# Kernel tuning notes

Hardware: AMD Instinct MI355X
Metric: run time of the kernel (lower is better)

Reference implementation:

```python
import jax, jax.numpy as jnp
import numpy as np

B, N, H = 512, 128, 256      # graphs, nodes per graph, hidden
NH, HD = 8, 32               # heads, head dim
DEG = 8
E = B * N * DEG              # 524288 edges
BN_EPS = 1e-5


def setup_inputs() -> dict:
    key = jax.random.key(0)
    ks = jax.random.split(key, 16)

    def w(k, shape):
        return jax.random.normal(k, shape, dtype=jnp.float32) * 0.02

    # intra-graph random edges: base offset per graph, local src/dst in [0, N)
    base = jnp.repeat(jnp.arange(B, dtype=jnp.int32) * N, N * DEG)
    edge_src = base + jax.random.randint(ks[1], (E,), 0, N, dtype=jnp.int32)
    edge_dst = base + jax.random.randint(ks[2], (E,), 0, N, dtype=jnp.int32)

    return {
        "h": jax.random.normal(ks[0], (B * N, H), dtype=jnp.float32),
        "edge_src": edge_src,
        "edge_dst": edge_dst,
        "gin_w1": w(ks[3], (H, H)), "gin_b1": jnp.zeros((H,), jnp.float32),
        "gin_w2": w(ks[4], (H, H)), "gin_b2": jnp.zeros((H,), jnp.float32),
        "attn_in_w": w(ks[5], (3 * H, H)), "attn_in_b": jnp.zeros((3 * H,), jnp.float32),
        "attn_out_w": w(ks[6], (H, H)), "attn_out_b": jnp.zeros((H,), jnp.float32),
        "bn_local_g": jnp.ones((H,), jnp.float32), "bn_local_b": jnp.zeros((H,), jnp.float32),
        "bn_attn_g": jnp.ones((H,), jnp.float32), "bn_attn_b": jnp.zeros((H,), jnp.float32),
        "bn_out_g": jnp.ones((H,), jnp.float32), "bn_out_b": jnp.zeros((H,), jnp.float32),
        "ffn1_w": w(ks[7], (2 * H, H)), "ffn1_b": jnp.zeros((2 * H,), jnp.float32),
        "ffn2_w": w(ks[8], (H, 2 * H)), "ffn2_b": jnp.zeros((H,), jnp.float32),
    }


def _bn(x, g, b):
    # nn.BatchNorm1d training-mode forward: batch stats over node dim, biased var
    mean = jnp.mean(x, axis=0)
    var = jnp.mean(jnp.square(x - mean), axis=0)
    return g * (x - mean) * jax.lax.rsqrt(var + BN_EPS) + b


def _mha(x, in_w, in_b, out_w, out_b):
    # x: [B, N, H]; uniform graphs -> key_padding_mask is all-valid
    qkv = x @ in_w.T + in_b                           # [B, N, 3H]
    q, k, v = jnp.split(qkv, 3, axis=-1)
    def heads(t):
        return t.reshape(B, N, NH, HD).transpose(0, 2, 1, 3)  # [B, NH, N, HD]
    q, k, v = heads(q), heads(k), heads(v)
    scores = jnp.einsum('bhqd,bhkd->bhqk', q, k) / jnp.sqrt(jnp.float32(HD))
    att = jax.nn.softmax(scores, axis=-1)
    o = jnp.einsum('bhqk,bhkd->bhqd', att, v).transpose(0, 2, 1, 3).reshape(B, N, H)
    return o @ out_w.T + out_b


def reference(h, edge_src, edge_dst,
              gin_w1, gin_b1, gin_w2, gin_b2,
              attn_in_w, attn_in_b, attn_out_w, attn_out_b,
              bn_local_g, bn_local_b, bn_attn_g, bn_attn_b, bn_out_g, bn_out_b,
              ffn1_w, ffn1_b, ffn2_w, ffn2_b):
    # --- local GIN branch: (1+eps)*h + sum_{j in N(i)} h_j, eps=0, then 2-layer MLP
    agg = jax.ops.segment_sum(h[edge_src], edge_dst, num_segments=B * N)
    z = h + agg
    h_local = jax.nn.relu(z @ gin_w1.T + gin_b1) @ gin_w2.T + gin_b2
    h_local = _bn(h + h_local, bn_local_g, bn_local_b)

    # --- global attention branch (to_dense_batch is an exact reshape here)
    h_dense = h.reshape(B, N, H)
    h_attn = _mha(h_dense, attn_in_w, attn_in_b, attn_out_w, attn_out_b).reshape(B * N, H)
    h_attn = _bn(h + h_attn, bn_attn_g, bn_attn_b)

    # --- combine + FFN + out norm
    x = h_local + h_attn
    x = x + jax.nn.relu(x @ ffn1_w.T + ffn1_b) @ ffn2_w.T + ffn2_b
    return _bn(x, bn_out_g, bn_out_b)
```

## Files before the change

### kernel.cpp

```cpp
#include <hip/hip_runtime.h>
#include <hip/hip_bf16.h>

#define B_   512
#define N_   128
#define H_   256
#define NH_  8
#define HD_  32
#define DEG_ 8
#define R_   (B_ * N_)
#define E_   (B_ * N_ * DEG_)
#define EPG_ (N_ * DEG_)

typedef unsigned short u16;
typedef unsigned int u32;

typedef __attribute__((ext_vector_type(8))) short s16x8;
typedef __attribute__((ext_vector_type(4))) float f32x4;

__device__ __forceinline__ float b2f(u16 u) {
  union { u32 i; float f; } v;
  v.i = ((u32)u) << 16;
  return v.f;
}
__device__ __forceinline__ u16 f2b(float f) {
// ... 33 lines not shown
#define OFF_F2B 657408
#define W_TOTAL 657664

__global__ __launch_bounds__(256) void prep_kernel(
    const float* __restrict__ hsrc, u16* __restrict__ hdst,
    const float* s0, const float* s1, const float* s2, const float* s3,
    const float* s4, const float* s5, const float* s6, const float* s7,
    const float* s8, const float* s9, const float* s10, const float* s11,
    u16* __restrict__ wdst, float* __restrict__ stats) {
  const int b = blockIdx.x, t = threadIdx.x;
  if (b < 16384) {
    const int e = (b * 256 + t) * 4;
    const float4 v = *(const float4*)(hsrc + e);
    ushort4 o;
    o.x = f2b(v.x); o.y = f2b(v.y); o.z = f2b(v.z); o.w = f2b(v.w);
    *(ushort4*)(hdst + tix(e >> 8, e & 255)) = o;
  } else if (b < 16384 + 643) {
    const int sizes[12] = {65536, 256, 65536, 256, 196608, 768,
                           65536, 256, 131072, 512, 131072, 256};
    const float* srcs[12] = {s0, s1, s2, s3, s4, s5, s6, s7, s8, s9, s10, s11};
    int gid = ((b - 16384) * 256 + t) * 4;
    if (gid >= W_TOTAL) return;
    int seg = 0, off = gid;
    while (off >= sizes[seg]) { off -= sizes[seg]; seg++; }
    const float4 v = *(const float4*)(srcs[seg] + off);
    ushort4 o;
    o.x = f2b(v.x); o.y = f2b(v.y); o.z = f2b(v.z); o.w = f2b(v.w);
    *(ushort4*)(wdst + gid) = o;
  } else {
    stats[(b - (16384 + 643)) * 256 + t] = 0.f;
  }
}

#define SROWS_ 32

__global__ __launch_bounds__(256) void agg_kernel(
    const u16* __restrict__ h, const int* __restrict__ esrc,
    const int* __restrict__ edst, u16* __restrict__ z) {
  __shared__ int s_src[EPG_];
  __shared__ int s_cnt[SROWS_];
  __shared__ int s_off[SROWS_ + 1];
  __shared__ int s_pos[SROWS_];
  const int g = blockIdx.x;
  const int r0 = blockIdx.y * SROWS_;
  const int t = threadIdx.x;

  if (t < SROWS_) s_cnt[t] = 0;
  __syncthreads();

  const int ebase = g * EPG_;
  int dl[4], sg[4];
#pragma unroll
  for (int i = 0; i < 4; i++) {
    const int e = ebase + t + i * 256;
    sg[i] = esrc[e];
    dl[i] = edst[e] - g * N_ - r0;
    if ((unsigned)dl[i] < SROWS_) atomicAdd(&s_cnt[dl[i]], 1);
  }
  __syncthreads();
  if (t == 0) {
    int acc = 0;
#pragma unroll
    for (int i = 0; i < SROWS_; i++) { s_off[i] = acc; acc += s_cnt[i]; }
    s_off[SROWS_] = acc;
  }
  __syncthreads();
  if (t < SROWS_) s_pos[t] = s_off[t];
  __syncthreads();
#pragma unroll
  for (int i = 0; i < 4; i++) {
    if ((unsigned)dl[i] < SROWS_) {
      const int slot = atomicAdd(&s_pos[dl[i]], 1);
      s_src[slot] = sg[i];
    }
  }
  __syncthreads();

  const int rg = t >> 5;
  const int c0 = (t & 31) * 8;
  for (int ib = 0; ib < SROWS_; ib += 8) {
    const int i = ib + rg;
    const int row = g * N_ + r0 + i;
    float acc[8];
    {
      const s16x8 v = *(const s16x8*)(h + tix(row, c0));
#pragma unroll
      for (int j = 0; j < 8; j++) acc[j] = b2f((u16)v[j]);
    }
    const int e0 = s_off[i], e1 = s_off[i + 1];
    for (int e = e0; e < e1; e++) {
      const int src = s_src[e];
      const s16x8 v = *(const s16x8*)(h + tix(src, c0));
#pragma unroll
      for (int j = 0; j < 8; j++) acc[j] += b2f((u16)v[j]);
    }
    s16x8 o;
#pragma unroll
    for (int j = 0; j < 8; j++) o[j] = (short)f2b(acc[j]);
    *(s16x8*)(z + tix(row, c0)) = o;
  }
}

template <int NC, int K, int RELU, int RES, int STATS, int ASPLIT, int CMODE>
__global__ __launch_bounds__(256) void gemm_mfma(
    const u16* A, const u16* A2,
    const u16* __restrict__ W, const u16* __restrict__ bias,
    const u16* res, u16* C0, u16* C1, u16* C2,
    float* __restrict__ gsum, float* __restrict__ gsq) {
  __shared__ u16 As[2][64 * 64] __attribute__((aligned(16)));
  __shared__ u16 Bs[2][64 * 64] __attribute__((aligned(16)));

  const int t = threadIdx.x;
  const int wave = t >> 6, lane = t & 63;
  const int wr = wave >> 1, wc = wave & 1;
  const int quad = lane >> 4, ln15 = lane & 15;
  const int row0 = blockIdx.y * 64, col0 = blockIdx.x * 64;

  f32x4 acc[2][2];
#pragma unroll
  for (int i = 0; i < 2; i++)
#pragma unroll
    for (int j = 0; j < 2; j++) acc[i][j] = (f32x4){0.f, 0.f, 0.f, 0.f};

  auto stage = [&](int b, int kt) {
    const u16* Ab;
    int ksl;
    if (ASPLIT) {
      if (kt < 256) { Ab = A; ksl = kt >> 6; } else { Ab = A2; ksl = (kt - 256) >> 6; }
    } else {
      Ab = A; ksl = kt >> 6;
    }
    const u16* abase = Ab + ((size_t)(row0 >> 7) << 15) + (ksl << 13) +
                       ((row0 & 64) << 6);
#pragma unroll
    for (int i = 0; i < 2; i++) {
      const int fid = t + i * 256;
      glds16(abase + fid * 8, &As[b][fid * 8]);
      const int row = fid >> 3;
      const int segp = (fid & 7) ^ (row & 7);
      glds16(W + (size_t)(col0 + row) * K + kt + segp * 8, &Bs[b][fid * 8]);
    }
  };

  stage(0, 0);
  for (int kt = 0; kt < K; kt += 64) {
    const int cur = (kt >> 6) & 1;
    if (kt + 64 < K) {
      stage(cur ^ 1, kt + 64);
      asm volatile("s_waitcnt vmcnt(4)" ::: "memory");
    } else {
      asm volatile("s_waitcnt vmcnt(0)" ::: "memory");
    }
    __builtin_amdgcn_s_barrier();
#pragma unroll
    for (int ks = 0; ks < 64; ks += 32) {
      s16x8 af[2], bf[2];
#pragma unroll
      for (int i = 0; i < 2; i++) {
        const int ra = wr * 32 + i * 16 + ln15;
        af[i] = *(const s16x8*)(
            &As[cur][ra * 64 + ((((ks >> 3) + quad) ^ (ra & 7)) * 8)]);
      }
#pragma unroll
      for (int j = 0; j < 2; j++) {
        const int rb = wc * 32 + j * 16 + ln15;
        bf[j] = *(const s16x8*)(
            &Bs[cur][rb * 64 + ((((ks >> 3) + quad) ^ (rb & 7)) * 8)]);
      }
#pragma unroll
      for (int i = 0; i < 2; i++)
#pragma unroll
        for (int j = 0; j < 2; j++)
          acc[i][j] = __builtin_amdgcn_mfma_f32_16x16x32_bf16(af[i], bf[j], acc[i][j], 0, 0, 0);
    }
    __builtin_amdgcn_s_barrier();
  }

  const int cbase = col0 + wc * 32;
  u16* Cb;
  int coff;
  if (CMODE) {
    const int chunk = col0 >> 8;
    Cb = (chunk == 0) ? C0 : ((chunk == 1) ? C1 : C2);
    coff = (col0 & 255) + wc * 32;
  } else {
    Cb = C0; coff = cbase;
  }

  float bs[2];
#pragma unroll
  for (int j = 0; j < 2; j++) bs[j] = b2f(bias[cbase + j * 16 + ln15]);

  float ssum[2] = {}, ssq[2] = {};
#pragma unroll
  for (int i = 0; i < 2; i++) {
    const int rbase = row0 + wr * 32 + i * 16 + quad * 4;
#pragma unroll
    for (int reg = 0; reg < 4; reg++) {
      const int row = rbase + reg;
#pragma unroll
      for (int j = 0; j < 2; j++) {
        float val = acc[i][j][reg] + bs[j];
        if (RELU) val = fmaxf(val, 0.f);
        if (RES) val += b2f(res[tix(row, cbase + j * 16 + ln15)]);
        Cb[tix(row, coff + j * 16 + ln15)] = f2b(val);
        if (STATS) { ssum[j] += val; ssq[j] += val * val; }
      }
    }
  }

  if (STATS) {
#pragma unroll
    for (int j = 0; j < 2; j++) {
      float s = ssum[j];
      s += __shfl_xor(s, 16);
      s += __shfl_xor(s, 32);
      float q = ssq[j];
      q += __shfl_xor(q, 16);
      q += __shfl_xor(q, 32);
      if (lane < 16) {
        atomicAdd(&gsum[cbase + j * 16 + lane], s);
        atomicAdd(&gsq[cbase + j * 16 + lane], q);
      }
    }
  }
}

__global__ __launch_bounds__(256) void qkv_mfma(
    const u16* A, const u16* __restrict__ W, const u16* __restrict__ bias,
    u16* Cq, u16* Ck, u16* Cv) {
  __shared__ u16 As[2][64 * 64] __attribute__((aligned(16)));
  __shared__ u16 Bs[2][3 * 64 * 64] __attribute__((aligned(16)));

  const int t = threadIdx.x;
  const int wave = t >> 6, lane = t & 63;
  const int wr = wave >> 1, wc = wave & 1;
  const int quad = lane >> 4, ln15 = lane & 15;
  const int row0 = blockIdx.y * 64, col0 = blockIdx.x * 64;

  f32x4 acc[3][2][2];
#pragma unroll
  for (int o = 0; o < 3; o++)
#pragma unroll
    for (int i = 0; i < 2; i++)
#pragma unroll
      for (int j = 0; j < 2; j++) acc[o][i][j] = (f32x4){0.f, 0.f, 0.f, 0.f};

  auto stage = [&](int b, int kt) {
    const u16* abase = A + ((size_t)(row0 >> 7) << 15) + ((kt >> 6) << 13) +
                       ((row0 & 64) << 6);
#pragma unroll
    for (int i = 0; i < 2; i++) {
      const int fid = t + i * 256;
      glds16(abase + fid * 8, &As[b][fid * 8]);
    }
#pragma unroll
    for (int o = 0; o < 3; o++)
#pragma unroll
      for (int i = 0; i < 2; i++) {
        const int fid = t + i * 256;
        const int row = fid >> 3;
        const int segp = (fid & 7) ^ (row & 7);
        glds16(W + (size_t)(o * 256 + col0 + row) * 256 + kt + segp * 8,
               &Bs[b][o * 4096 + fid * 8]);
      }
  };

  stage(0, 0);
  for (int kt = 0; kt < 256; kt += 64) {
    const int cur = (kt >> 6) & 1;
    if (kt + 64 < 256) {
      stage(cur ^ 1, kt + 64);
      asm volatile("s_waitcnt vmcnt(8)" ::: "memory");
    } else {
      asm volatile("s_waitcnt vmcnt(0)" ::: "memory");
    }
    __builtin_amdgcn_s_barrier();
#pragma unroll
    for (int ks = 0; ks < 64; ks += 32) {
      s16x8 af[2];
#pragma unroll
      for (int i = 0; i < 2; i++) {
        const int ra = wr * 32 + i * 16 + ln15;
        af[i] = *(const s16x8*)(
            &As[cur][ra * 64 + ((((ks >> 3) + quad) ^ (ra & 7)) * 8)]);
      }
#pragma unroll
      for (int o = 0; o < 3; o++) {
        s16x8 bf[2];
#pragma unroll
        for (int j = 0; j < 2; j++) {
          const int rb = wc * 32 + j * 16 + ln15;
          bf[j] = *(const s16x8*)(
              &Bs[cur][o * 4096 + rb * 64 + ((((ks >> 3) + quad) ^ (rb & 7)) * 8)]);
        }
#pragma unroll
        for (int i = 0; i < 2; i++)
#pragma unroll
          for (int j = 0; j < 2; j++)
            acc[o][i][j] = __builtin_amdgcn_mfma_f32_16x16x32_bf16(af[i], bf[j], acc[o][i][j], 0, 0, 0);
      }
    }
    __builtin_amdgcn_s_barrier();
  }

  const int cbase = col0 + wc * 32;
#pragma unroll
  for (int o = 0; o < 3; o++) {
    u16* Co = (o == 0) ? Cq : ((o == 1) ? Ck : Cv);
    float bs[2];
#pragma unroll
    for (int j = 0; j < 2; j++) bs[j] = b2f(bias[o * 256 + cbase + j * 16 + ln15]);
#pragma unroll
    for (int i = 0; i < 2; i++) {
      const int rbase = row0 + wr * 32 + i * 16 + quad * 4;
#pragma unroll
      for (int reg = 0; reg < 4; reg++) {
        const int row = rbase + reg;
#pragma unroll
        for (int j = 0; j < 2; j++)
          Co[tix(row, cbase + j * 16 + ln15)] = f2b(acc[o][i][j][reg] + bs[j]);
      }
    }
  }
}

template <int CHUNKS, int RES_LDS, int COMBINE>
__global__ __launch_bounds__(256, 2) void fused_mlp(
    const u16* A, const u16* Ara,
    const u16* __restrict__ W1, const u16* __restrict__ b1,
    const u16* __restrict__ W2, const u16* __restrict__ b2,
    const u16* resg, u16* C, const float* __restrict__ st,
    const float* __restrict__ bn0g, const float* __restrict__ bn0b,
    const float* __restrict__ bn1g, const float* __restrict__ bn1b,
    float* __restrict__ gsum, float* __restrict__ gsq) {
  __shared__ u16 xs[4 * 64 * 64] __attribute__((aligned(16)));
  __shared__ u16 tc[64 * 128] __attribute__((aligned(16)));
  __shared__ u16 Wst[2][128 * 64] __attribute__((aligned(16)));

  const int t = threadIdx.x;
  const int wave = t >> 6, lane = t & 63;
  const int wr = wave >> 1, wc = wave & 1;
  const int quad = lane >> 4, ln15 = lane & 15;
  const int row0 = blockIdx.x * 64;
  const int K2 = CHUNKS * 128;

  if (COMBINE) {
    float* cf = (float*)tc;
    {
      const float ml = st[t] * (1.f / R_);
      const float vl = fmaxf(st[256 + t] * (1.f / R_) - ml * ml, 0.f);
      const float al = bn0g[t] * rsqrtf(vl + 1e-5f);
      cf[t] = al;
      cf[256 + t] = bn0b[t] - ml * al;
// ... 177 lines not shown
      const int rowl = wr * 32 + i * 16 + quad * 4 + reg;
      const int row = row0 + rowl;
#pragma unroll
      for (int j = 0; j < 8; j++) {
        const int col = wc * 128 + j * 16 + ln15;
        float val = acc2[i][j][reg] + bs2[j];
        if (RES_LDS) {
          val += b2f(xs[(col >> 6) * 4096 + rowl * 64 +
                        ((((col >> 3) & 7) ^ (rowl & 7)) << 3) + (col & 7)]);
        } else {
          val += b2f(resg[tix(row, col)]);
        }
        C[tix(row, col)] = f2b(val);
        ssum[j] += val; ssq[j] += val * val;
      }
    }
  }

#pragma unroll
  for (int j = 0; j < 8; j++) {
    float s = ssum[j];
    s += __shfl_xor(s, 16);
    s += __shfl_xor(s, 32);
    float q = ssq[j];
    q += __shfl_xor(q, 16);
    q += __shfl_xor(q, 32);
    if (lane < 16) {
      atomicAdd(&gsum[wc * 128 + j * 16 + lane], s);
      atomicAdd(&gsq[wc * 128 + j * 16 + lane], q);
    }
  }
}

__global__ __launch_bounds__(256) void attn_mfma(
    const u16* q, const u16* __restrict__ k,
    const u16* __restrict__ v, u16* o) {
  __shared__ u16 lds[21760] __attribute__((aligned(16)));
  u16* Vt = lds;
  u16* Qs = lds + 4352;
  u16* Ks = lds + 4352 + 5120;
  u16* P  = lds + 4352;

  const int g = blockIdx.x >> 3;
  const int hd = blockIdx.x & 7;
  const int t = threadIdx.x;
  const int wave = t >> 6, lane = t & 63;
  const int quad = lane >> 4, ln15 = lane & 15;
  const int strip = wave * 32;
  const float scale = 0.1767766952966369f;

#pragma unroll
  for (int i = 0; i < 4; i++) {
    const int fid = t + i * 256;
    const int row = fid >> 3;
    const int seg = fid & 7;
    const int gidx = tix(g * N_ + row, hd * HD_ + seg * 4);
    const ushort4 qv = *(const ushort4*)(q + gidx);
    const ushort4 kv = *(const ushort4*)(k + gidx);
    const ushort4 vv = *(const ushort4*)(v + gidx);
    ushort4 qs;
    qs.x = f2b(b2f(qv.x) * scale); qs.y = f2b(b2f(qv.y) * scale);
    qs.z = f2b(b2f(qv.z) * scale); qs.w = f2b(b2f(qv.w) * scale);
    *(ushort4*)(Qs + row * 40 + seg * 4) = qs;
    *(ushort4*)(Ks + row * 40 + seg * 4) = kv;
    Vt[(seg * 4 + 0) * 136 + row] = vv.x;
    Vt[(seg * 4 + 1) * 136 + row] = vv.y;
    Vt[(seg * 4 + 2) * 136 + row] = vv.z;
    Vt[(seg * 4 + 3) * 136 + row] = vv.w;
  }
  __syncthreads();

  s16x8 af[2], bf[8];
#pragma unroll
  for (int mi = 0; mi < 2; mi++)
    af[mi] = *(const s16x8*)(Qs + (strip + mi * 16 + ln15) * 40 + quad * 8);
#pragma unroll
  for (int nj = 0; nj < 8; nj++)
    bf[nj] = *(const s16x8*)(Ks + (nj * 16 + ln15) * 40 + quad * 8);

  f32x4 acc[2][8];
#pragma unroll
  for (int mi = 0; mi < 2; mi++)
#pragma unroll
    for (int nj = 0; nj < 8; nj++)
      acc[mi][nj] = __builtin_amdgcn_mfma_f32_16x16x32_bf16(
          af[mi], bf[nj], (f32x4){0.f, 0.f, 0.f, 0.f}, 0, 0, 0);

  __syncthreads();

#pragma unroll
  for (int mi = 0; mi < 2; mi++) {
#pragma unroll
    for (int reg = 0; reg < 4; reg++) {
      float mx = acc[mi][0][reg];
#pragma unroll
      for (int j = 1; j < 8; j++) mx = fmaxf(mx, acc[mi][j][reg]);
      mx = fmaxf(mx, __shfl_xor(mx, 1));
      mx = fmaxf(mx, __shfl_xor(mx, 2));
      mx = fmaxf(mx, __shfl_xor(mx, 4));
      mx = fmaxf(mx, __shfl_xor(mx, 8));
      float e[8], s = 0.f;
#pragma unroll
      for (int j = 0; j < 8; j++) { e[j] = __expf(acc[mi][j][reg] - mx); s += e[j]; }
      s += __shfl_xor(s, 1);
      s += __shfl_xor(s, 2);
      s += __shfl_xor(s, 4);
      s += __shfl_xor(s, 8);
      const float inv = 1.f / s;
      const int prow = strip + mi * 16 + quad * 4 + reg;
#pragma unroll
      for (int j = 0; j < 8; j++)
        P[prow * 136 + j * 16 + ln15] = f2b(e[j] * inv);
    }
  }
  __syncthreads();

  f32x4 acc2[2][2];
#pragma unroll
  for (int mi = 0; mi < 2; mi++)
#pragma unroll
    for (int nj = 0; nj < 2; nj++) acc2[mi][nj] = (f32x4){0.f, 0.f, 0.f, 0.f};
#pragma unroll
  for (int kt = 0; kt < 4; kt++) {
    s16x8 paf[2], vbf[2];
#pragma unroll
    for (int mi = 0; mi < 2; mi++)
      paf[mi] = *(const s16x8*)(P + (strip + mi * 16 + ln15) * 136 + kt * 32 + quad * 8);
#pragma unroll
    for (int nj = 0; nj < 2; nj++)
      vbf[nj] = *(const s16x8*)(Vt + (nj * 16 + ln15) * 136 + kt * 32 + quad * 8);
#pragma unroll
    for (int mi = 0; mi < 2; mi++)
#pragma unroll
      for (int nj = 0; nj < 2; nj++)
        acc2[mi][nj] = __builtin_amdgcn_mfma_f32_16x16x32_bf16(
            paf[mi], vbf[nj], acc2[mi][nj], 0, 0, 0);
  }

#pragma unroll
  for (int mi = 0; mi < 2; mi++)
#pragma unroll
    for (int nj = 0; nj < 2; nj++)
#pragma unroll
      for (int reg = 0; reg < 4; reg++) {
        const int row = strip + mi * 16 + quad * 4 + reg;
        o[tix(g * N_ + row, hd * HD_ + nj * 16 + ln15)] =
            f2b(acc2[mi][nj][reg]);
      }
}

__global__ __launch_bounds__(256) void final_kernel(
    const u16* __restrict__ y, const float* __restrict__ st,
    const float* __restrict__ bg, const float* __restrict__ bb,
    float* __restrict__ out) {
  const int e = (blockIdx.x * 256 + threadIdx.x) * 4;
  const int col = e & 255;
  float y4[4];
  ld4b(y + tix(e >> 8, col), y4);
  const float4 s4 = *(const float4*)(st + 1024 + col);
  const float4 q4 = *(const float4*)(st + 1280 + col);
  const float4 g4 = *(const float4*)(bg + col);
  const float4 b4 = *(const float4*)(bb + col);
  const float ss[4] = {s4.x, s4.y, s4.z, s4.w};
  const float qq[4] = {q4.x, q4.y, q4.z, q4.w};
  const float gg[4] = {g4.x, g4.y, g4.z, g4.w};
  const float bv[4] = {b4.x, b4.y, b4.z, b4.w};
  float4 o;
  float* ov = (float*)&o;
#pragma unroll
  for (int j = 0; j < 4; j++) {
    const float mean = ss[j] * (1.f / R_);
    const float var = fmaxf(qq[j] * (1.f / R_) - mean * mean, 0.f);
    const float a = gg[j] * rsqrtf(var + 1e-5f);
    ov[j] = a * y4[j] + (bv[j] - mean * a);
  }
  *(float4*)(out + e) = o;
}

extern "C" void kernel_launch(void* const* d_in, const int* in_sizes, int n_in,
                              void* d_out, int out_size, void* d_ws, size_t ws_size,
                              hipStream_t stream) {
  const float* h = (const float*)d_in[0];
  const int* esrc = (const int*)d_in[1];
  const int* edst = (const int*)d_in[2];
  const float* bn_local_g = (const float*)d_in[11];
  const float* bn_local_b = (const float*)d_in[12];
  const float* bn_attn_g = (const float*)d_in[13];
  const float* bn_attn_b = (const float*)d_in[14];
  const float* bn_out_g = (const float*)d_in[15];
  const float* bn_out_b = (const float*)d_in[16];

  const size_t RH = (size_t)R_ * H_;
  float* stats = (float*)d_ws;
  u16* WB = (u16*)((char*)d_ws + 65536);
  u16* Hb = (u16*)((char*)d_ws + 65536 + 2097152);
  u16* S1 = Hb + RH;
  u16* S2 = S1 + RH;
  u16* OD = (u16*)d_out;
  float* outf = (float*)d_out;

  prep_kernel<<<16384 + 643 + 12, 256, 0, stream>>>(
      h, Hb,
      (const float*)d_in[3], (const float*)d_in[4], (const float*)d_in[5],
      (const float*)d_in[6], (const float*)d_in[7], (const float*)d_in[8],
      (const float*)d_in[9], (const float*)d_in[10], (const float*)d_in[17],
      (const float*)d_in[18], (const float*)d_in[19], (const float*)d_in[20],
      WB, stats);

  qkv_mfma<<<dim3(4, 1024), 256, 0, stream>>>(
      Hb, WB + OFF_AIW, WB + OFF_AIB, S1, S2, OD);
  attn_mfma<<<B_ * NH_, 256, 0, stream>>>(S1, S2, OD, S1);
  gemm_mfma<256, 256, 0, 1, 1, 0, 0><<<dim3(4, 1024), 256, 0, stream>>>(
      S1, nullptr, WB + OFF_AOW, WB + OFF_AOB, Hb, S2, nullptr, nullptr,
      stats + 512, stats + 768);
  agg_kernel<<<dim3(B_, 4), 256, 0, stream>>>(Hb, esrc, edst, OD);
  fused_mlp<2, 0, 0><<<1024, 256, 0, stream>>>(
      OD, nullptr,
      WB + OFF_GW1, WB + OFF_GB1, WB + OFF_GW2, WB + OFF_GB2,
      Hb, OD, nullptr, nullptr, nullptr, nullptr, nullptr,
      stats + 0, stats + 256);
  fused_mlp<4, 1, 1><<<1024, 256, 0, stream>>>(
      OD, S2,
      WB + OFF_F1W, WB + OFF_F1B, WB + OFF_F2W, WB + OFF_F2B,
      nullptr, S1, stats, bn_local_g, bn_local_b, bn_attn_g, bn_attn_b,
      stats + 1024, stats + 1280);
  final_kernel<<<(int)(RH / 4 / 256), 256, 0, stream>>>(
      S1, stats, bn_out_g, bn_out_b, outf);
}
```

Measured before the change: 532.5 us.

## Merge independent branch kernels into horizontally fused launches

Attention and GIN neighbor aggregation now share one launch that dispatches on block index, and the GIN MLP and attention output projection share a second launch. Aggregation output goes to a separate buffer (OD2) so the two branches no longer conflict over OD. The goal is to cut launch count and let independent work from the two branches fill the GPU together, reducing tail and launch overhead. The cost is larger LDS and register footprints in the merged kernels, which may lower occupancy (launch_bounds 256,2 on gin_ao).

```diff
diff --git a/kernel.cpp b/kernel.cpp
--- a/kernel.cpp
+++ b/kernel.cpp
@@ -89,83 +89,11 @@
   }
 }
 
-#define SROWS_ 32
-
-__global__ __launch_bounds__(256) void agg_kernel(
-    const u16* __restrict__ h, const int* __restrict__ esrc,
-    const int* __restrict__ edst, u16* __restrict__ z) {
-  __shared__ int s_src[EPG_];
-  __shared__ int s_cnt[SROWS_];
-  __shared__ int s_off[SROWS_ + 1];
-  __shared__ int s_pos[SROWS_];
-  const int g = blockIdx.x;
-  const int r0 = blockIdx.y * SROWS_;
-  const int t = threadIdx.x;
-
-  if (t < SROWS_) s_cnt[t] = 0;
-  __syncthreads();
-
-  const int ebase = g * EPG_;
-  int dl[4], sg[4];
-#pragma unroll
-  for (int i = 0; i < 4; i++) {
-    const int e = ebase + t + i * 256;
-    sg[i] = esrc[e];
-    dl[i] = edst[e] - g * N_ - r0;
-    if ((unsigned)dl[i] < SROWS_) atomicAdd(&s_cnt[dl[i]], 1);
-  }
-  __syncthreads();
-  if (t == 0) {
-    int acc = 0;
-#pragma unroll
-    for (int i = 0; i < SROWS_; i++) { s_off[i] = acc; acc += s_cnt[i]; }
-    s_off[SROWS_] = acc;
-  }
-  __syncthreads();
-  if (t < SROWS_) s_pos[t] = s_off[t];
-  __syncthreads();
-#pragma unroll
-  for (int i = 0; i < 4; i++) {
-    if ((unsigned)dl[i] < SROWS_) {
-      const int slot = atomicAdd(&s_pos[dl[i]], 1);
-      s_src[slot] = sg[i];
-    }
-  }
-  __syncthreads();
-
-  const int rg = t >> 5;
-  const int c0 = (t & 31) * 8;
-  for (int ib = 0; ib < SROWS_; ib += 8) {
-    const int i = ib + rg;
-    const int row = g * N_ + r0 + i;
-    float acc[8];
-    {
-      const s16x8 v = *(const s16x8*)(h + tix(row, c0));
-#pragma unroll
-      for (int j = 0; j < 8; j++) acc[j] = b2f((u16)v[j]);
-    }
-    const int e0 = s_off[i], e1 = s_off[i + 1];
-    for (int e = e0; e < e1; e++) {
-      const int src = s_src[e];
-      const s16x8 v = *(const s16x8*)(h + tix(src, c0));
-#pragma unroll
-      for (int j = 0; j < 8; j++) acc[j] += b2f((u16)v[j]);
-    }
-    s16x8 o;
-#pragma unroll
-    for (int j = 0; j < 8; j++) o[j] = (short)f2b(acc[j]);
-    *(s16x8*)(z + tix(row, c0)) = o;
-  }
-}
-
-template <int NC, int K, int RELU, int RES, int STATS, int ASPLIT, int CMODE>
-__global__ __launch_bounds__(256) void gemm_mfma(
-    const u16* A, const u16* A2,
-    const u16* __restrict__ W, const u16* __restrict__ bias,
-    const u16* res, u16* C0, u16* C1, u16* C2,
-    float* __restrict__ gsum, float* __restrict__ gsq) {
+__global__ __launch_bounds__(256) void qkv_mfma(
+    const u16* A, const u16* __restrict__ W, const u16* __restrict__ bias,
+    u16* Cq, u16* Ck, u16* Cv) {
   __shared__ u16 As[2][64 * 64] __attribute__((aligned(16)));
-  __shared__ u16 Bs[2][64 * 64] __attribute__((aligned(16)));
+  __shared__ u16 Bs[2][3 * 64 * 64] __attribute__((aligned(16)));
 
   const int t = threadIdx.x;
   const int wave = t >> 6, lane = t & 63;
@@ -173,45 +101,47 @@
   const int quad = lane >> 4, ln15 = lane & 15;
   const int row0 = blockIdx.y * 64, col0 = blockIdx.x * 64;
 
-  f32x4 acc[2][2];
-#pragma unroll
-  for (int i = 0; i < 2; i++)
-#pragma unroll
-    for (int j = 0; j < 2; j++) acc[i][j] = (f32x4){0.f, 0.f, 0.f, 0.f};
+  f32x4 acc[3][2][2];
+#pragma unroll
+  for (int o = 0; o < 3; o++)
+#pragma unroll
+    for (int i = 0; i < 2; i++)
+#pragma unroll
+      for (int j = 0; j < 2; j++) acc[o][i][j] = (f32x4){0.f, 0.f, 0.f, 0.f};
 
   auto stage = [&](int b, int kt) {
-    const u16* Ab;
-    int ksl;
-    if (ASPLIT) {
-      if (kt < 256) { Ab = A; ksl = kt >> 6; } else { Ab = A2; ksl = (kt - 256) >> 6; }
-    } else {
-      Ab = A; ksl = kt >> 6;
-    }
-    const u16* abase = Ab + ((size_t)(row0 >> 7) << 15) + (ksl << 13) +
+    const u16* abase = A + ((size_t)(row0 >> 7) << 15) + ((kt >> 6) << 13) +
                        ((row0 & 64) << 6);
 #pragma unroll
     for (int i = 0; i < 2; i++) {
       const int fid = t + i * 256;
       glds16(abase + fid * 8, &As[b][fid * 8]);
-      const int row = fid >> 3;
-      const int segp = (fid & 7) ^ (row & 7);
-      glds16(W + (size_t)(col0 + row) * K + kt + segp * 8, &Bs[b][fid * 8]);
-    }
+    }
+#pragma unroll
+    for (int o = 0; o < 3; o++)
+#pragma unroll
+      for (int i = 0; i < 2; i++) {
+        const int fid = t + i * 256;
+        const int row = fid >> 3;
+        const int segp = (fid & 7) ^ (row & 7);
+        glds16(W + (size_t)(o * 256 + col0 + row) * 256 + kt + segp * 8,
+               &Bs[b][o * 4096 + fid * 8]);
+      }
   };
 
   stage(0, 0);
-  for (int kt = 0; kt < K; kt += 64) {
+  for (int kt = 0; kt < 256; kt += 64) {
     const int cur = (kt >> 6) & 1;
-    if (kt + 64 < K) {
+    if (kt + 64 < 256) {
       stage(cur ^ 1, kt + 64);
-      asm volatile("s_waitcnt vmcnt(4)" ::: "memory");
+      asm volatile("s_waitcnt vmcnt(8)" ::: "memory");
     } else {
       asm volatile("s_waitcnt vmcnt(0)" ::: "memory");
     }
     __builtin_amdgcn_s_barrier();
 #pragma unroll
     for (int ks = 0; ks < 64; ks += 32) {
-      s16x8 af[2], bf[2];
+      s16x8 af[2];
 #pragma unroll
       for (int i = 0; i < 2; i++) {
         const int ra = wr * 32 + i * 16 + ln15;
@@ -219,54 +149,496 @@
             &As[cur][ra * 64 + ((((ks >> 3) + quad) ^ (ra & 7)) * 8)]);
       }
 #pragma unroll
-      for (int j = 0; j < 2; j++) {
-        const int rb = wc * 32 + j * 16 + ln15;
-        bf[j] = *(const s16x8*)(
-            &Bs[cur][rb * 64 + ((((ks >> 3) + quad) ^ (rb & 7)) * 8)]);
-      }
-#pragma unroll
-      for (int i = 0; i < 2; i++)
-#pragma unroll
-        for (int j = 0; j < 2; j++)
-          acc[i][j] = __builtin_amdgcn_mfma_f32_16x16x32_bf16(af[i], bf[j], acc[i][j], 0, 0, 0);
+      for (int o = 0; o < 3; o++) {
+        s16x8 bf[2];
+#pragma unroll
+        for (int j = 0; j < 2; j++) {
+          const int rb = wc * 32 + j * 16 + ln15;
+          bf[j] = *(const s16x8*)(
+              &Bs[cur][o * 4096 + rb * 64 + ((((ks >> 3) + quad) ^ (rb & 7)) * 8)]);
+        }
+#pragma unroll
+        for (int i = 0; i < 2; i++)
+#pragma unroll
+          for (int j = 0; j < 2; j++)
+            acc[o][i][j] = __builtin_amdgcn_mfma_f32_16x16x32_bf16(af[i], bf[j], acc[o][i][j], 0, 0, 0);
+      }
     }
     __builtin_amdgcn_s_barrier();
   }
 
   const int cbase = col0 + wc * 32;
-  u16* Cb;
-  int coff;
-  if (CMODE) {
-    const int chunk = col0 >> 8;
-    Cb = (chunk == 0) ? C0 : ((chunk == 1) ? C1 : C2);
-    coff = (col0 & 255) + wc * 32;
+#pragma unroll
+  for (int o = 0; o < 3; o++) {
+    u16* Co = (o == 0) ? Cq : ((o == 1) ? Ck : Cv);
+    float bs[2];
+#pragma unroll
+    for (int j = 0; j < 2; j++) bs[j] = b2f(bias[o * 256 + cbase + j * 16 + ln15]);
+#pragma unroll
+    for (int i = 0; i < 2; i++) {
+      const int rbase = row0 + wr * 32 + i * 16 + quad * 4;
+#pragma unroll
+      for (int reg = 0; reg < 4; reg++) {
+        const int row = rbase + reg;
+#pragma unroll
+        for (int j = 0; j < 2; j++)
+          Co[tix(row, cbase + j * 16 + ln15)] = f2b(acc[o][i][j][reg] + bs[j]);
+      }
+    }
+  }
+}
+
+__global__ __launch_bounds__(256) void attn_agg(
+    const u16* q, const u16* __restrict__ k,
+    const u16* __restrict__ v, u16* o,
+    const u16* __restrict__ h, const int* __restrict__ esrc,
+    const int* __restrict__ edst, u16* __restrict__ z) {
+  __shared__ u16 lds[21760] __attribute__((aligned(16)));
+  const int t = threadIdx.x;
+
+  if (blockIdx.x < 4096) {
+    u16* Vt = lds;
+    u16* Qs = lds + 4352;
+    u16* Ks = lds + 4352 + 5120;
+    u16* P  = lds + 4352;
+
+    const int g = blockIdx.x >> 3;
+    const int hd = blockIdx.x & 7;
+    const int wave = t >> 6, lane = t & 63;
+    const int quad = lane >> 4, ln15 = lane & 15;
+    const int strip = wave * 32;
+    const float scale = 0.1767766952966369f;
+
+#pragma unroll
+    for (int i = 0; i < 4; i++) {
+      const int fid = t + i * 256;
+      const int row = fid >> 3;
+      const int seg = fid & 7;
+      const int gidx = tix(g * N_ + row, hd * HD_ + seg * 4);
+      const ushort4 qv = *(const ushort4*)(q + gidx);
+      const ushort4 kv = *(const ushort4*)(k + gidx);
+      const ushort4 vv = *(const ushort4*)(v + gidx);
+      ushort4 qs;
+      qs.x = f2b(b2f(qv.x) * scale); qs.y = f2b(b2f(qv.y) * scale);
+      qs.z = f2b(b2f(qv.z) * scale); qs.w = f2b(b2f(qv.w) * scale);
+      *(ushort4*)(Qs + row * 40 + seg * 4) = qs;
+      *(ushort4*)(Ks + row * 40 + seg * 4) = kv;
+      Vt[(seg * 4 + 0) * 136 + row] = vv.x;
+      Vt[(seg * 4 + 1) * 136 + row] = vv.y;
+      Vt[(seg * 4 + 2) * 136 + row] = vv.z;
+      Vt[(seg * 4 + 3) * 136 + row] = vv.w;
+    }
+    __syncthreads();
+
+    s16x8 af[2], bf[8];
+#pragma unroll
+    for (int mi = 0; mi < 2; mi++)
+      af[mi] = *(const s16x8*)(Qs + (strip + mi * 16 + ln15) * 40 + quad * 8);
+#pragma unroll
+    for (int nj = 0; nj < 8; nj++)
+      bf[nj] = *(const s16x8*)(Ks + (nj * 16 + ln15) * 40 + quad * 8);
+
+    f32x4 acc[2][8];
+#pragma unroll
+    for (int mi = 0; mi < 2; mi++)
+#pragma unroll
+      for (int nj = 0; nj < 8; nj++)
+        acc[mi][nj] = __builtin_amdgcn_mfma_f32_16x16x32_bf16(
+            af[mi], bf[nj], (f32x4){0.f, 0.f, 0.f, 0.f}, 0, 0, 0);
+
+    __syncthreads();
+
+#pragma unroll
+    for (int mi = 0; mi < 2; mi++) {
+#pragma unroll
+      for (int reg = 0; reg < 4; reg++) {
+        float mx = acc[mi][0][reg];
+#pragma unroll
+        for (int j = 1; j < 8; j++) mx = fmaxf(mx, acc[mi][j][reg]);
+        mx = fmaxf(mx, __shfl_xor(mx, 1));
+        mx = fmaxf(mx, __shfl_xor(mx, 2));
+        mx = fmaxf(mx, __shfl_xor(mx, 4));
+        mx = fmaxf(mx, __shfl_xor(mx, 8));
+        float e[8], s = 0.f;
+#pragma unroll
+        for (int j = 0; j < 8; j++) { e[j] = __expf(acc[mi][j][reg] - mx); s += e[j]; }
+        s += __shfl_xor(s, 1);
+        s += __shfl_xor(s, 2);
+        s += __shfl_xor(s, 4);
+        s += __shfl_xor(s, 8);
+        const float inv = 1.f / s;
+        const int prow = strip + mi * 16 + quad * 4 + reg;
+#pragma unroll
+        for (int j = 0; j < 8; j++)
+          P[prow * 136 + j * 16 + ln15] = f2b(e[j] * inv);
+      }
+    }
+    __syncthreads();
+
+    f32x4 acc2[2][2];
+#pragma unroll
+    for (int mi = 0; mi < 2; mi++)
+#pragma unroll
+      for (int nj = 0; nj < 2; nj++) acc2[mi][nj] = (f32x4){0.f, 0.f, 0.f, 0.f};
+#pragma unroll
+    for (int kt = 0; kt < 4; kt++) {
+      s16x8 paf[2], vbf[2];
+#pragma unroll
+      for (int mi = 0; mi < 2; mi++)
+        paf[mi] = *(const s16x8*)(P + (strip + mi * 16 + ln15) * 136 + kt * 32 + quad * 8);
+#pragma unroll
+      for (int nj = 0; nj < 2; nj++)
+        vbf[nj] = *(const s16x8*)(Vt + (nj * 16 + ln15) * 136 + kt * 32 + quad * 8);
+#pragma unroll
+      for (int mi = 0; mi < 2; mi++)
+#pragma unroll
+        for (int nj = 0; nj < 2; nj++)
+          acc2[mi][nj] = __builtin_amdgcn_mfma_f32_16x16x32_bf16(
+              paf[mi], vbf[nj], acc2[mi][nj], 0, 0, 0);
+    }
+
+#pragma unroll
+    for (int mi = 0; mi < 2; mi++)
+#pragma unroll
+      for (int nj = 0; nj < 2; nj++)
+#pragma unroll
+        for (int reg = 0; reg < 4; reg++) {
+          const int row = strip + mi * 16 + quad * 4 + reg;
+          o[tix(g * N_ + row, hd * HD_ + nj * 16 + ln15)] =
+              f2b(acc2[mi][nj][reg]);
+        }
   } else {
-    Cb = C0; coff = cbase;
+    const int bid2 = blockIdx.x - 4096;
+    const int g = bid2 & 511;
+    const int r0 = (bid2 >> 9) * 32;
+    int* s_src = (int*)lds;
+    int* s_cnt = (int*)(lds + 2048);
+    int* s_off = (int*)(lds + 2112);
+    int* s_pos = (int*)(lds + 2180);
+
+    if (t < 32) s_cnt[t] = 0;
+    __syncthreads();
+
+    const int ebase = g * EPG_;
+    int dl[4], sg[4];
+#pragma unroll
+    for (int i = 0; i < 4; i++) {
+      const int e = ebase + t + i * 256;
+      sg[i] = esrc[e];
+      dl[i] = edst[e] - g * N_ - r0;
+      if ((unsigned)dl[i] < 32u) atomicAdd(&s_cnt[dl[i]], 1);
+    }
+    __syncthreads();
+    if (t == 0) {
+      int acc = 0;
+#pragma unroll
+      for (int i = 0; i < 32; i++) { s_off[i] = acc; acc += s_cnt[i]; }
+      s_off[32] = acc;
+    }
+    __syncthreads();
+    if (t < 32) s_pos[t] = s_off[t];
+    __syncthreads();
+#pragma unroll
+    for (int i = 0; i < 4; i++) {
+      if ((unsigned)dl[i] < 32u) {
+        const int slot = atomicAdd(&s_pos[dl[i]], 1);
+        s_src[slot] = sg[i];
+      }
+    }
+    __syncthreads();
+
+    const int rg = t >> 5;
+    const int c0 = (t & 31) * 8;
+    for (int ib = 0; ib < 32; ib += 8) {
+      const int i = ib + rg;
+      const int row = g * N_ + r0 + i;
+      float acc[8];
+      {
+        const s16x8 vv = *(const s16x8*)(h + tix(row, c0));
+#pragma unroll
+        for (int j = 0; j < 8; j++) acc[j] = b2f((u16)vv[j]);
+      }
+      const int e0 = s_off[i], e1 = s_off[i + 1];
+      for (int e = e0; e < e1; e++) {
+        const int src = s_src[e];
+        const s16x8 vv = *(const s16x8*)(h + tix(src, c0));
+#pragma unroll
+        for (int j = 0; j < 8; j++) acc[j] += b2f((u16)vv[j]);
+      }
+      s16x8 ov;
+#pragma unroll
+      for (int j = 0; j < 8; j++) ov[j] = (short)f2b(acc[j]);
+      *(s16x8*)(z + tix(row, c0)) = ov;
+    }
   }
-
-  float bs[2];
-#pragma unroll
-  for (int j = 0; j < 2; j++) bs[j] = b2f(bias[cbase + j * 16 + ln15]);
-
-  float ssum[2] = {}, ssq[2] = {};
-#pragma unroll
-  for (int i = 0; i < 2; i++) {
-    const int rbase = row0 + wr * 32 + i * 16 + quad * 4;
-#pragma unroll
-    for (int reg = 0; reg < 4; reg++) {
-      const int row = rbase + reg;
-#pragma unroll
-      for (int j = 0; j < 2; j++) {
-        float val = acc[i][j][reg] + bs[j];
-        if (RELU) val = fmaxf(val, 0.f);
-        if (RES) val += b2f(res[tix(row, cbase + j * 16 + ln15)]);
-        Cb[tix(row, coff + j * 16 + ln15)] = f2b(val);
-        if (STATS) { ssum[j] += val; ssq[j] += val * val; }
-      }
-    }
-  }
-
-  if (STATS) {
+}
+
+__global__ __launch_bounds__(256, 2) void gin_ao(
+    const u16* zA, const u16* __restrict__ gres,
+    const u16* __restrict__ GW1, const u16* __restrict__ GB1,
+    const u16* __restrict__ GW2, const u16* __restrict__ GB2,
+    u16* Cgin, float* __restrict__ gsum_l, float* __restrict__ gsq_l,
+    const u16* Aao, const u16* __restrict__ AOW, const u16* __restrict__ AOB,
+    const u16* __restrict__ ares, u16* Cao,
+    float* __restrict__ gsum_a, float* __restrict__ gsq_a) {
+  __shared__ u16 shbuf[40960] __attribute__((aligned(16)));
+  const int t = threadIdx.x;
+  const int wave = t >> 6, lane = t & 63;
+  const int wr = wave >> 1, wc = wave & 1;
+  const int quad = lane >> 4, ln15 = lane & 15;
+
+  if (blockIdx.x < 1024) {
+    u16* xs = shbuf;
+    u16* tc = shbuf + 16384;
+    const int row0 = blockIdx.x * 64;
+
+    {
+      const u16* abase = zA + ((size_t)(row0 >> 7) << 15) + ((row0 & 64) << 6);
+#pragma unroll
+      for (int i = 0; i < 8; i++) {
+        const int gid = t + i * 256;
+        const int kstep = gid >> 9;
+        const int fid = gid & 511;
+        glds16(abase + kstep * 8192 + fid * 8, xs + gid * 8);
+      }
+    }
+
+    f32x4 acc2[2][8];
+#pragma unroll
+    for (int i = 0; i < 2; i++)
+#pragma unroll
+      for (int j = 0; j < 8; j++) acc2[i][j] = (f32x4){0.f, 0.f, 0.f, 0.f};
+
+    auto tca = [&](int row, int col) {
+      const int s0 = col >> 3;
+      return row * 128 + (((s0 & 8) | ((s0 ^ row) & 7)) << 3) + (col & 7);
+    };
+
+    for (int c = 0; c < 2; c++) {
+      f32x4 acc1[2][4];
+#pragma unroll
+      for (int i = 0; i < 2; i++)
+#pragma unroll
+        for (int j = 0; j < 4; j++) acc1[i][j] = (f32x4){0.f, 0.f, 0.f, 0.f};
+
+      auto stage1 = [&](int b, int kt) {
+#pragma unroll
+        for (int i = 0; i < 4; i++) {
+          const int fid = t + i * 256;
+          const int row = fid >> 3;
+          const int segp = (fid & 7) ^ (row & 7);
+          glds16(GW1 + (size_t)(c * 128 + row) * 256 + kt + segp * 8,
+                 shbuf + 24576 + b * 8192 + fid * 8);
+        }
+      };
+
+      stage1(0, 0);
+      for (int kt = 0; kt < 256; kt += 64) {
+        const int cur = (kt >> 6) & 1;
+        if (kt + 64 < 256) {
+          stage1(cur ^ 1, kt + 64);
+          asm volatile("s_waitcnt vmcnt(4)" ::: "memory");
+        } else {
+          asm volatile("s_waitcnt vmcnt(0)" ::: "memory");
+        }
+        __builtin_amdgcn_s_barrier();
+#pragma unroll
+        for (int ks = 0; ks < 64; ks += 32) {
+          s16x8 af[2], bf[4];
+#pragma unroll
+          for (int i = 0; i < 2; i++) {
+            const int ra = wr * 32 + i * 16 + ln15;
+            af[i] = *(const s16x8*)(
+                &xs[(kt >> 6) * 4096 + ra * 64 +
+                    ((((ks >> 3) + quad) ^ (ra & 7)) * 8)]);
+          }
+#pragma unroll
+          for (int j = 0; j < 4; j++) {
+            const int rb = wc * 64 + j * 16 + ln15;
+            bf[j] = *(const s16x8*)(
+                shbuf + 24576 + cur * 8192 + rb * 64 +
+                ((((ks >> 3) + quad) ^ (rb & 7)) * 8));
+          }
+#pragma unroll
+          for (int i = 0; i < 2; i++)
+#pragma unroll
+            for (int j = 0; j < 4; j++)
+              acc1[i][j] = __builtin_amdgcn_mfma_f32_16x16x32_bf16(af[i], bf[j], acc1[i][j], 0, 0, 0);
+        }
+        __builtin_amdgcn_s_barrier();
+      }
+
+      {
+        float b1s[4];
+#pragma unroll
+        for (int j = 0; j < 4; j++)
+          b1s[j] = b2f(GB1[c * 128 + wc * 64 + j * 16 + ln15]);
+#pragma unroll
+        for (int i = 0; i < 2; i++)
+#pragma unroll
+          for (int reg = 0; reg < 4; reg++) {
+            const int rowl = wr * 32 + i * 16 + quad * 4 + reg;
+#pragma unroll
+            for (int j = 0; j < 4; j++) {
+              const int coll = wc * 64 + j * 16 + ln15;
+              tc[tca(rowl, coll)] = f2b(fmaxf(acc1[i][j][reg] + b1s[j], 0.f));
+            }
+          }
+      }
+      __syncthreads();
+
+      for (int ks2 = 0; ks2 < 2; ks2++) {
+#pragma unroll
+        for (int i = 0; i < 8; i++) {
+          const int fid = t + i * 256;
+          const int row = fid >> 3;
+          const int segp = (fid & 7) ^ (row & 7);
+          glds16(GW2 + (size_t)row * 256 + c * 128 + ks2 * 64 + segp * 8,
+                 shbuf + 24576 + fid * 8);
+        }
+        asm volatile("s_waitcnt vmcnt(0)" ::: "memory");
+        __builtin_amdgcn_s_barrier();
+#pragma unroll
+        for (int ksl = 0; ksl < 64; ksl += 32) {
+          s16x8 af[2], bf[8];
+#pragma unroll
+          for (int i = 0; i < 2; i++) {
+            const int ra = wr * 32 + i * 16 + ln15;
+            af[i] = *(const s16x8*)(&tc[tca(ra, ks2 * 64 + ksl + quad * 8)]);
+          }
+#pragma unroll
+          for (int j = 0; j < 8; j++) {
+            const int rb = wc * 128 + j * 16 + ln15;
+            bf[j] = *(const s16x8*)(
+                shbuf + 24576 + rb * 64 + ((((ksl >> 3) + quad) ^ (rb & 7)) * 8));
+          }
+#pragma unroll
+          for (int i = 0; i < 2; i++)
+#pragma unroll
+            for (int j = 0; j < 8; j++)
+              acc2[i][j] = __builtin_amdgcn_mfma_f32_16x16x32_bf16(af[i], bf[j], acc2[i][j], 0, 0, 0);
+        }
+        __builtin_amdgcn_s_barrier();
+      }
+    }
+
+    float bs2[8];
+#pragma unroll
+    for (int j = 0; j < 8; j++)
+      bs2[j] = b2f(GB2[wc * 128 + j * 16 + ln15]);
+
+    float ssum[8] = {}, ssq[8] = {};
+#pragma unroll
+    for (int i = 0; i < 2; i++) {
+#pragma unroll
+      for (int reg = 0; reg < 4; reg++) {
+        const int rowl = wr * 32 + i * 16 + quad * 4 + reg;
+        const int row = row0 + rowl;
+#pragma unroll
+        for (int j = 0; j < 8; j++) {
+          const int col = wc * 128 + j * 16 + ln15;
+          float val = acc2[i][j][reg] + bs2[j];
+          val += b2f(gres[tix(row, col)]);
+          Cgin[tix(row, col)] = f2b(val);
+          ssum[j] += val; ssq[j] += val * val;
+        }
+      }
+    }
+
+#pragma unroll
+    for (int j = 0; j < 8; j++) {
+      float s = ssum[j];
+      s += __shfl_xor(s, 16);
+      s += __shfl_xor(s, 32);
+      float q = ssq[j];
+      q += __shfl_xor(q, 16);
+      q += __shfl_xor(q, 32);
+      if (lane < 16) {
+        atomicAdd(&gsum_l[wc * 128 + j * 16 + lane], s);
+        atomicAdd(&gsq_l[wc * 128 + j * 16 + lane], q);
+      }
+    }
+  } else {
+    const int bid2 = blockIdx.x - 1024;
+    const int col0 = (bid2 & 3) * 64;
+    const int row0 = (bid2 >> 2) * 64;
+
+    f32x4 acc[2][2];
+#pragma unroll
+    for (int i = 0; i < 2; i++)
+#pragma unroll
+      for (int j = 0; j < 2; j++) acc[i][j] = (f32x4){0.f, 0.f, 0.f, 0.f};
+
+    auto stage = [&](int b, int kt) {
+      const u16* abase = Aao + ((size_t)(row0 >> 7) << 15) + ((kt >> 6) << 13) +
+                         ((row0 & 64) << 6);
+#pragma unroll
+      for (int i = 0; i < 2; i++) {
+        const int fid = t + i * 256;
+        glds16(abase + fid * 8, shbuf + b * 4096 + fid * 8);
+        const int row = fid >> 3;
+        const int segp = (fid & 7) ^ (row & 7);
+        glds16(AOW + (size_t)(col0 + row) * 256 + kt + segp * 8,
+               shbuf + 8192 + b * 4096 + fid * 8);
+      }
+    };
+
+    stage(0, 0);
+    for (int kt = 0; kt < 256; kt += 64) {
+      const int cur = (kt >> 6) & 1;
+      if (kt + 64 < 256) {
+        stage(cur ^ 1, kt + 64);
+        asm volatile("s_waitcnt vmcnt(4)" ::: "memory");
+      } else {
+        asm volatile("s_waitcnt vmcnt(0)" ::: "memory");
+      }
+      __builtin_amdgcn_s_barrier();
+#pragma unroll
+      for (int ks = 0; ks < 64; ks += 32) {
+        s16x8 af[2], bf[2];
+#pragma unroll
+        for (int i = 0; i < 2; i++) {
+          const int ra = wr * 32 + i * 16 + ln15;
+          af[i] = *(const s16x8*)(
+              shbuf + cur * 4096 + ra * 64 + ((((ks >> 3) + quad) ^ (ra & 7)) * 8));
+        }
+#pragma unroll
+        for (int j = 0; j < 2; j++) {
+          const int rb = wc * 32 + j * 16 + ln15;
+          bf[j] = *(const s16x8*)(
+              shbuf + 8192 + cur * 4096 + rb * 64 + ((((ks >> 3) + quad) ^ (rb & 7)) * 8));
+        }
+#pragma unroll
+        for (int i = 0; i < 2; i++)
+#pragma unroll
+          for (int j = 0; j < 2; j++)
+            acc[i][j] = __builtin_amdgcn_mfma_f32_16x16x32_bf16(af[i], bf[j], acc[i][j], 0, 0, 0);
+      }
+      __builtin_amdgcn_s_barrier();
+    }
+
+    const int cbase = col0 + wc * 32;
+    float bs[2];
+#pragma unroll
+    for (int j = 0; j < 2; j++) bs[j] = b2f(AOB[cbase + j * 16 + ln15]);
+
+    float ssum[2] = {}, ssq[2] = {};
+#pragma unroll
+    for (int i = 0; i < 2; i++) {
+      const int rbase = row0 + wr * 32 + i * 16 + quad * 4;
+#pragma unroll
+      for (int reg = 0; reg < 4; reg++) {
+        const int row = rbase + reg;
+#pragma unroll
+        for (int j = 0; j < 2; j++) {
+          float val = acc[i][j][reg] + bs[j];
+          val += b2f(ares[tix(row, cbase + j * 16 + ln15)]);
+          Cao[tix(row, cbase + j * 16 + ln15)] = f2b(val);
+          ssum[j] += val; ssq[j] += val * val;
+        }
+      }
+    }
+
 #pragma unroll
     for (int j = 0; j < 2; j++) {
       float s = ssum[j];
@@ -276,107 +648,8 @@
       q += __shfl_xor(q, 16);
       q += __shfl_xor(q, 32);
       if (lane < 16) {
-        atomicAdd(&gsum[cbase + j * 16 + lane], s);
-        atomicAdd(&gsq[cbase + j * 16 + lane], q);
-      }
-    }
-  }
-}
-
-__global__ __launch_bounds__(256) void qkv_mfma(
-    const u16* A, const u16* __restrict__ W, const u16* __restrict__ bias,
-    u16* Cq, u16* Ck, u16* Cv) {
-  __shared__ u16 As[2][64 * 64] __attribute__((aligned(16)));
-  __shared__ u16 Bs[2][3 * 64 * 64] __attribute__((aligned(16)));
-
-  const int t = threadIdx.x;
-  const int wave = t >> 6, lane = t & 63;
-  const int wr = wave >> 1, wc = wave & 1;
-  const int quad = lane >> 4, ln15 = lane & 15;
-  const int row0 = blockIdx.y * 64, col0 = blockIdx.x * 64;
-
-  f32x4 acc[3][2][2];
-#pragma unroll
-  for (int o = 0; o < 3; o++)
-#pragma unroll
-    for (int i = 0; i < 2; i++)
-#pragma unroll
-      for (int j = 0; j < 2; j++) acc[o][i][j] = (f32x4){0.f, 0.f, 0.f, 0.f};
-
-  auto stage = [&](int b, int kt) {
-    const u16* abase = A + ((size_t)(row0 >> 7) << 15) + ((kt >> 6) << 13) +
-                       ((row0 & 64) << 6);
-#pragma unroll
-    for (int i = 0; i < 2; i++) {
-      const int fid = t + i * 256;
-      glds16(abase + fid * 8, &As[b][fid * 8]);
-    }
-#pragma unroll
-    for (int o = 0; o < 3; o++)
-#pragma unroll
-      for (int i = 0; i < 2; i++) {
-        const int fid = t + i * 256;
-        const int row = fid >> 3;
-        const int segp = (fid & 7) ^ (row & 7);
-        glds16(W + (size_t)(o * 256 + col0 + row) * 256 + kt + segp * 8,
-               &Bs[b][o * 4096 + fid * 8]);
-      }
-  };
-
-  stage(0, 0);
-  for (int kt = 0; kt < 256; kt += 64) {
-    const int cur = (kt >> 6) & 1;
-    if (kt + 64 < 256) {
-      stage(cur ^ 1, kt + 64);
-      asm volatile("s_waitcnt vmcnt(8)" ::: "memory");
-    } else {
-      asm volatile("s_waitcnt vmcnt(0)" ::: "memory");
-    }
-    __builtin_amdgcn_s_barrier();
-#pragma unroll
-    for (int ks = 0; ks < 64; ks += 32) {
-      s16x8 af[2];
-#pragma unroll
-      for (int i = 0; i < 2; i++) {
-        const int ra = wr * 32 + i * 16 + ln15;
-        af[i] = *(const s16x8*)(
-            &As[cur][ra * 64 + ((((ks >> 3) + quad) ^ (ra & 7)) * 8)]);
-      }
-#pragma unroll
-      for (int o = 0; o < 3; o++) {
-        s16x8 bf[2];
-#pragma unroll
-        for (int j = 0; j < 2; j++) {
-          const int rb = wc * 32 + j * 16 + ln15;
-          bf[j] = *(const s16x8*)(
-              &Bs[cur][o * 4096 + rb * 64 + ((((ks >> 3) + quad) ^ (rb & 7)) * 8)]);
-        }
-#pragma unroll
-        for (int i = 0; i < 2; i++)
-#pragma unroll
-          for (int j = 0; j < 2; j++)
-            acc[o][i][j] = __builtin_amdgcn_mfma_f32_16x16x32_bf16(af[i], bf[j], acc[o][i][j], 0, 0, 0);
-      }
-    }
-    __builtin_amdgcn_s_barrier();
-  }
-
-  const int cbase = col0 + wc * 32;
-#pragma unroll
-  for (int o = 0; o < 3; o++) {
-    u16* Co = (o == 0) ? Cq : ((o == 1) ? Ck : Cv);
-    float bs[2];
-#pragma unroll
-    for (int j = 0; j < 2; j++) bs[j] = b2f(bias[o * 256 + cbase + j * 16 + ln15]);
-#pragma unroll
-    for (int i = 0; i < 2; i++) {
-      const int rbase = row0 + wr * 32 + i * 16 + quad * 4;
-#pragma unroll
-      for (int reg = 0; reg < 4; reg++) {
-        const int row = rbase + reg;
-#pragma unroll
-        for (int j = 0; j < 2; j++)
-          Co[tix(row, cbase + j * 16 + ln15)] = f2b(acc[o][i][j][reg] + bs[j]);
+        atomicAdd(&gsum_a[cbase + j * 16 + lane], s);
+        atomicAdd(&gsq_a[cbase + j * 16 + lane], q);
       }
     }
   }
@@ -620,123 +893,6 @@
   }
 }
 
-__global__ __launch_bounds__(256) void attn_mfma(
-    const u16* q, const u16* __restrict__ k,
-    const u16* __restrict__ v, u16* o) {
-  __shared__ u16 lds[21760] __attribute__((aligned(16)));
-  u16* Vt = lds;
-  u16* Qs = lds + 4352;
-  u16* Ks = lds + 4352 + 5120;
-  u16* P  = lds + 4352;
-
-  const int g = blockIdx.x >> 3;
-  const int hd = blockIdx.x & 7;
-  const int t = threadIdx.x;
-  const int wave = t >> 6, lane = t & 63;
-  const int quad = lane >> 4, ln15 = lane & 15;
-  const int strip = wave * 32;
-  const float scale = 0.1767766952966369f;
-
-#pragma unroll
-  for (int i = 0; i < 4; i++) {
-    const int fid = t + i * 256;
-    const int row = fid >> 3;
-    const int seg = fid & 7;
-    const int gidx = tix(g * N_ + row, hd * HD_ + seg * 4);
-    const ushort4 qv = *(const ushort4*)(q + gidx);
-    const ushort4 kv = *(const ushort4*)(k + gidx);
-    const ushort4 vv = *(const ushort4*)(v + gidx);
-    ushort4 qs;
-    qs.x = f2b(b2f(qv.x) * scale); qs.y = f2b(b2f(qv.y) * scale);
-    qs.z = f2b(b2f(qv.z) * scale); qs.w = f2b(b2f(qv.w) * scale);
-    *(ushort4*)(Qs + row * 40 + seg * 4) = qs;
-    *(ushort4*)(Ks + row * 40 + seg * 4) = kv;
-    Vt[(seg * 4 + 0) * 136 + row] = vv.x;
-    Vt[(seg * 4 + 1) * 136 + row] = vv.y;
-    Vt[(seg * 4 + 2) * 136 + row] = vv.z;
-    Vt[(seg * 4 + 3) * 136 + row] = vv.w;
-  }
-  __syncthreads();
-
-  s16x8 af[2], bf[8];
-#pragma unroll
-  for (int mi = 0; mi < 2; mi++)
-    af[mi] = *(const s16x8*)(Qs + (strip + mi * 16 + ln15) * 40 + quad * 8);
-#pragma unroll
-  for (int nj = 0; nj < 8; nj++)
-    bf[nj] = *(const s16x8*)(Ks + (nj * 16 + ln15) * 40 + quad * 8);
-
-  f32x4 acc[2][8];
-#pragma unroll
-  for (int mi = 0; mi < 2; mi++)
-#pragma unroll
-    for (int nj = 0; nj < 8; nj++)
-      acc[mi][nj] = __builtin_amdgcn_mfma_f32_16x16x32_bf16(
-          af[mi], bf[nj], (f32x4){0.f, 0.f, 0.f, 0.f}, 0, 0, 0);
-
-  __syncthreads();
-
-#pragma unroll
-  for (int mi = 0; mi < 2; mi++) {
-#pragma unroll
-    for (int reg = 0; reg < 4; reg++) {
-      float mx = acc[mi][0][reg];
-#pragma unroll
-      for (int j = 1; j < 8; j++) mx = fmaxf(mx, acc[mi][j][reg]);
-      mx = fmaxf(mx, __shfl_xor(mx, 1));
-      mx = fmaxf(mx, __shfl_xor(mx, 2));
-      mx = fmaxf(mx, __shfl_xor(mx, 4));
-      mx = fmaxf(mx, __shfl_xor(mx, 8));
-      float e[8], s = 0.f;
-#pragma unroll
-      for (int j = 0; j < 8; j++) { e[j] = __expf(acc[mi][j][reg] - mx); s += e[j]; }
-      s += __shfl_xor(s, 1);
-      s += __shfl_xor(s, 2);
-      s += __shfl_xor(s, 4);
-      s += __shfl_xor(s, 8);
-      const float inv = 1.f / s;
-      const int prow = strip + mi * 16 + quad * 4 + reg;
-#pragma unroll
-      for (int j = 0; j < 8; j++)
-        P[prow * 136 + j * 16 + ln15] = f2b(e[j] * inv);
-    }
-  }
-  __syncthreads();
-
-  f32x4 acc2[2][2];
-#pragma unroll
-  for (int mi = 0; mi < 2; mi++)
-#pragma unroll
-    for (int nj = 0; nj < 2; nj++) acc2[mi][nj] = (f32x4){0.f, 0.f, 0.f, 0.f};
-#pragma unroll
-  for (int kt = 0; kt < 4; kt++) {
-    s16x8 paf[2], vbf[2];
-#pragma unroll
-    for (int mi = 0; mi < 2; mi++)
-      paf[mi] = *(const s16x8*)(P + (strip + mi * 16 + ln15) * 136 + kt * 32 + quad * 8);
-#pragma unroll
-    for (int nj = 0; nj < 2; nj++)
-      vbf[nj] = *(const s16x8*)(Vt + (nj * 16 + ln15) * 136 + kt * 32 + quad * 8);
-#pragma unroll
-    for (int mi = 0; mi < 2; mi++)
-#pragma unroll
-      for (int nj = 0; nj < 2; nj++)
-        acc2[mi][nj] = __builtin_amdgcn_mfma_f32_16x16x32_bf16(
-            paf[mi], vbf[nj], acc2[mi][nj], 0, 0, 0);
-  }
-
-#pragma unroll
-  for (int mi = 0; mi < 2; mi++)
-#pragma unroll
-    for (int nj = 0; nj < 2; nj++)
-#pragma unroll
-      for (int reg = 0; reg < 4; reg++) {
-        const int row = strip + mi * 16 + quad * 4 + reg;
-        o[tix(g * N_ + row, hd * HD_ + nj * 16 + ln15)] =
-            f2b(acc2[mi][nj][reg]);
-      }
-}
-
 __global__ __launch_bounds__(256) void final_kernel(
     const u16* __restrict__ y, const float* __restrict__ st,
     const float* __restrict__ bg, const float* __restrict__ bb,
@@ -785,6 +941,7 @@
   u16* S1 = Hb + RH;
   u16* S2 = S1 + RH;
   u16* OD = (u16*)d_out;
+  u16* OD2 = OD + RH;
   float* outf = (float*)d_out;
 
   prep_kernel<<<16384 + 643 + 12, 256, 0, stream>>>(
@@ -797,16 +954,12 @@
 
   qkv_mfma<<<dim3(4, 1024), 256, 0, stream>>>(
       Hb, WB + OFF_AIW, WB + OFF_AIB, S1, S2, OD);
-  attn_mfma<<<B_ * NH_, 256, 0, stream>>>(S1, S2, OD, S1);
-  gemm_mfma<256, 256, 0, 1, 1, 0, 0><<<dim3(4, 1024), 256, 0, stream>>>(
-      S1, nullptr, WB + OFF_AOW, WB + OFF_AOB, Hb, S2, nullptr, nullptr,
-      stats + 512, stats + 768);
-  agg_kernel<<<dim3(B_, 4), 256, 0, stream>>>(Hb, esrc, edst, OD);
-  fused_mlp<2, 0, 0><<<1024, 256, 0, stream>>>(
-      OD, nullptr,
-      WB + OFF_GW1, WB + OFF_GB1, WB + OFF_GW2, WB + OFF_GB2,
-      Hb, OD, nullptr, nullptr, nullptr, nullptr, nullptr,
-      stats + 0, stats + 256);
+  attn_agg<<<4096 + 2048, 256, 0, stream>>>(
+      S1, S2, OD, S1, Hb, esrc, edst, OD2);
+  gin_ao<<<1024 + 4096, 256, 0, stream>>>(
+      OD2, Hb, WB + OFF_GW1, WB + OFF_GB1, WB + OFF_GW2, WB + OFF_GB2,
+      OD, stats + 0, stats + 256,
+      S1, WB + OFF_AOW, WB + OFF_AOB, Hb, S2, stats + 512, stats + 768);
   fused_mlp<4, 1, 1><<<1024, 256, 0, stream>>>(
       OD, S2,
       WB + OFF_F1W, WB + OFF_F1B, WB + OFF_F2W, WB + OFF_F2B,
```

New measurement: 522.3 us. Within noise of the previous version (-1.9%).
